# Kernel tuning notes

Hardware: AMD Instinct MI355X
Metric: run time of the kernel (lower is better)

## Reference

```python
import jax, jax.numpy as jnp
import numpy as np


def setup_inputs() -> dict:
    key = jax.random.key(0)
    k1, k2, k3, k4 = jax.random.split(key, 4)
    B, L, R, H, D = 64, 512, 512, 512, 256
    return {
        "lstm_lt": jax.random.normal(k1, (B, L, H), dtype=jnp.float32),
        "lstm_rt": jax.random.normal(k2, (B, R, H), dtype=jnp.float32),
        "atten_W": jax.random.normal(k3, (H, D), dtype=jnp.float32) * 0.05,
        "diagnoal_W": jax.random.normal(k4, (1, 1, D), dtype=jnp.float32) * 0.05,
    }


def reference(lstm_lt, lstm_rt, atten_W, diagnoal_W):
    # Projection (the original's broadcast-multiply-sum is exactly a GEMM):
    # atten_lt[b,l,d] = tanh(sum_h lstm_lt[b,l,h] * W[h,d]) * diag_W[d]
    atten_lt = jnp.tanh(jnp.einsum('blh,hd->bld', lstm_lt, atten_W)) * diagnoal_W
    atten_rt = jnp.tanh(jnp.einsum('brh,hd->brd', lstm_rt, atten_W))
    # batch_dot over the attention dim -> (B, L, R)
    atten_value = jnp.einsum('bld,brd->blr', atten_lt, atten_rt)
    # No masks supplied (len(inputs)==2 path); softmax over last axis.
    return jax.nn.softmax(atten_value, axis=-1)
```

## Files before the change

kernel.cpp:

```cpp
#include <hip/hip_runtime.h>

typedef __attribute__((ext_vector_type(8))) __bf16 bf16x8;
typedef __attribute__((ext_vector_type(4))) float f32x4;

#define DI __device__ __forceinline__

DI unsigned short f2bf(float x) {
  unsigned u = __float_as_uint(x);
  u += 0x7fffu + ((u >> 16) & 1u);
  return (unsigned short)(u >> 16);
}

DI bf16x8 cvt8(f32x4 lo, f32x4 hi) {
  bf16x8 r;
  r[0] = (__bf16)lo.x; r[1] = (__bf16)lo.y; r[2] = (__bf16)lo.z; r[3] = (__bf16)lo.w;
  r[4] = (__bf16)hi.x; r[5] = (__bf16)hi.y; r[6] = (__bf16)hi.z; r[7] = (__bf16)hi.w;
  return r;
}

DI float tanh_fast(float x) {
  float ax = fabsf(x);
  float e = __expf(-2.0f * ax);
  float t = (1.0f - e) / (1.0f + e);
  return x < 0.0f ? -t : t;
}

DI void glds16(const void* gptr, void* lptr) {
  __builtin_amdgcn_global_load_lds(
      (const __attribute__((address_space(1))) unsigned int*)gptr,
      (__attribute__((address_space(3))) unsigned int*)lptr, 16, 0, 0);
}


__global__ void k_wt(const float* __restrict__ W, unsigned short* __restrict__ Wt) {
  int n  = blockIdx.x;
  int k8 = threadIdx.x;
  unsigned v[8];
#pragma unroll
  for (int j = 0; j < 8; j++) v[j] = f2bf(W[(k8 * 8 + j) * 256 + n]);
  uint4 p;
  p.x = v[0] | (v[1] << 16);
  p.y = v[2] | (v[3] << 16);
  p.z = v[4] | (v[5] << 16);
  p.w = v[6] | (v[7] << 16);
  size_t idx = ((size_t)(n >> 4) * 16 + (k8 >> 2)) * 512 + (k8 & 3) * 128 + (n & 15) * 8;
  *(uint4*)&Wt[idx] = p;
}

__global__ __launch_bounds__(512, 4) void k_proj(
    const float* __restrict__ Alt, const float* __restrict__ Art,
    const unsigned short* __restrict__ Wt, const float* __restrict__ diag,
    unsigned short* __restrict__ Olt, unsigned short* __restrict__ Ort) {
  __shared__ __align__(16) float As[128 * 64];

  int bx = blockIdx.x;
  bool is_lt = bx < 256;
  int m0 = (is_lt ? bx : bx - 256) * 128;
  const char* Abase = (const char*)((is_lt ? Alt : Art) + (size_t)m0 * 512);
  const char* Bt = (const char*)Wt;

  int tid  = threadIdx.x;
  int lane = tid & 63;
  int wid  = tid >> 6;
  int wm   = wid >> 2;
  int wn   = wid & 3;
  int l15  = lane & 15;
  int quad = lane >> 4;
  int r7   = l15 & 7;

  int lr4 = lane >> 4, c16 = lane & 15;
  int aoff = lr4 * 2048 + ((c16 ^ lr4) << 4);

  char* AsB = (char*)As;

  f32x4 zero = {0.0f, 0.0f, 0.0f, 0.0f};
  f32x4 acc[4][4];
#pragma unroll
  for (int i = 0; i < 4; i++)
#pragma unroll
    for (int j = 0; j < 4; j++) acc[i][j] = zero;

  for (int k0 = 0; k0 < 512; k0 += 64) {
    uint4 bv[2][4];
#pragma unroll
    for (int ks = 0; ks < 2; ks++)
#pragma unroll
      for (int nt = 0; nt < 4; nt++)
        bv[ks][nt] = *(const uint4*)(
            Bt + (((size_t)(wn * 4 + nt) * 16 + (k0 >> 5) + ks) << 10) + lane * 16);

#pragma unroll
    for (int i = 0; i < 4; i++) {
      int j = wid * 4 + i;
      glds16(Abase + (size_t)j * 8192 + (size_t)k0 * 4 + (aoff ^ ((j & 1) << 6)),
             AsB + j * 1024);
    }
    __syncthreads();

#pragma unroll
    for (int ks = 0; ks < 2; ks++) {
      bf16x8 a[4];
#pragma unroll
      for (int mt = 0; mt < 4; mt++) {
        int row = wm * 64 + mt * 16 + l15;
        int c0 = ks * 8 + quad * 2;
        f32x4 lo = *(const f32x4*)(AsB + row * 256 + (((c0    ) ^ r7) << 4));
        f32x4 hi = *(const f32x4*)(AsB + row * 256 + (((c0 + 1) ^ r7) << 4));
        a[mt] = cvt8(lo, hi);
      }
      __builtin_amdgcn_s_setprio(1);
#pragma unroll
      for (int mt = 0; mt < 4; mt++)
#pragma unroll
        for (int nt = 0; nt < 4; nt++)
          acc[mt][nt] = __builtin_amdgcn_mfma_f32_16x16x32_bf16(
              a[mt], __builtin_bit_cast(bf16x8, bv[ks][nt]), acc[mt][nt], 0, 0, 0);
      __builtin_amdgcn_s_setprio(0);
    }
    __syncthreads();
  }

  float dscale[4];
#pragma unroll
  for (int nt = 0; nt < 4; nt++)
    dscale[nt] = is_lt ? diag[wn * 64 + nt * 16 + l15] : 1.0f;

  if (is_lt) {
    unsigned short* O = Olt + (size_t)m0 * 256;
#pragma unroll
    for (int mt = 0; mt < 4; mt++)
#pragma unroll
      for (int r = 0; r < 4; r++) {
        int row = wm * 64 + mt * 16 + quad * 4 + r;
#pragma unroll
        for (int nt = 0; nt < 4; nt++) {
          int col = wn * 64 + nt * 16 + l15;
          O[(size_t)row * 256 + col] = f2bf(tanh_fast(acc[mt][nt][r]) * dscale[nt]);
        }
      }
  } else {
#pragma unroll
    for (int mt = 0; mt < 4; mt++)
#pragma unroll
      for (int r = 0; r < 4; r++) {
        int row = wm * 64 + mt * 16 + quad * 4 + r;
        int m = m0 + row;
        int bb = m >> 9, rr = m & 511;
#pragma unroll
        for (int nt = 0; nt < 4; nt++) {
          int d = wn * 64 + nt * 16 + l15;
          size_t idx = (size_t)bb * 131072 +
                       ((size_t)(rr >> 4) * 8 + (d >> 5)) * 512 +
                       ((d >> 3) & 3) * 128 + (rr & 15) * 8 + (d & 7);
          Ort[idx] = f2bf(tanh_fast(acc[mt][nt][r]));
        }
      }
  }
}

__global__ __launch_bounds__(512, 4) void k_attn(
    const unsigned short* __restrict__ Lt, const unsigned short* __restrict__ Rt,
    float* __restrict__ Out) {
  __shared__ __align__(16) unsigned short Ls[64 * 256];
  __shared__ float red[8][64];
  __shared__ float rowv[64];

  int bx = blockIdx.x;
  int b  = (bx & 7) * 8 + ((bx >> 3) & 7);
  int l0 = (bx >> 6) * 64;
  const char* Lb = (const char*)(Lt + ((size_t)b * 512 + l0) * 256);
  const char* Rb = (const char*)Rt + (size_t)b * 262144;
  float* Ob = Out + ((size_t)b * 512 + l0) * 512;

  int tid  = threadIdx.x;
  int lane = tid & 63;
  int wid  = tid >> 6;
  int l15  = lane & 15;
  int quad = lane >> 4;
  int r7   = l15 & 7;

  char* LsB = (char*)Ls;

  f32x4 zero = {0.0f, 0.0f, 0.0f, 0.0f};
  f32x4 acc[4][4];
#pragma unroll
  for (int i = 0; i < 4; i++)
#pragma unroll
    for (int j = 0; j < 4; j++) acc[i][j] = zero;

#pragma unroll
  for (int i = 0; i < 4; i++) {
    int grow = wid * 8 + i * 2 + (lane >> 5);
    glds16(Lb + (size_t)grow * 512 + (((lane & 31) ^ (grow & 7)) << 4),
           LsB + (wid * 8 + i * 2) * 512 + (lane & 31) * 16 + (lane >> 5) * 512);
  }
  __syncthreads();

  for (int t = 0; t < 8; t++) {
    uint4 rv[4];
#pragma unroll
    for (int nt = 0; nt < 4; nt++)
      rv[nt] = *(const uint4*)(
          Rb + (((size_t)(wid * 4 + nt) * 8 + t) << 10) + lane * 16);
    bf16x8 a[4];
#pragma unroll
    for (int mt = 0; mt < 4; mt++) {
      int row = mt * 16 + l15;
      a[mt] = *(const bf16x8*)(LsB + row * 512 + (((t * 4 + quad) ^ r7) << 4));
    }
    __builtin_amdgcn_s_setprio(1);
#pragma unroll
    for (int mt = 0; mt < 4; mt++)
#pragma unroll
      for (int nt = 0; nt < 4; nt++)
        acc[mt][nt] = __builtin_amdgcn_mfma_f32_16x16x32_bf16(
            a[mt], __builtin_bit_cast(bf16x8, rv[nt]), acc[mt][nt], 0, 0, 0);
    __builtin_amdgcn_s_setprio(0);
  }

#pragma unroll
  for (int mt = 0; mt < 4; mt++) {
#pragma unroll
    for (int r = 0; r < 4; r++) {
      float m = fmaxf(fmaxf(acc[mt][0][r], acc[mt][1][r]),
                      fmaxf(acc[mt][2][r], acc[mt][3][r]));
      m = fmaxf(m, __shfl_xor(m, 1));
      m = fmaxf(m, __shfl_xor(m, 2));
      m = fmaxf(m, __shfl_xor(m, 4));
      m = fmaxf(m, __shfl_xor(m, 8));
      if (l15 == 0) red[wid][mt * 16 + quad * 4 + r] = m;
    }
  }
  __syncthreads();
  if (tid < 64) {
    float m = red[0][tid];
#pragma unroll
    for (int w = 1; w < 8; w++) m = fmaxf(m, red[w][tid]);
    rowv[tid] = m;
  }
  __syncthreads();

#pragma unroll
  for (int mt = 0; mt < 4; mt++) {
#pragma unroll
    for (int r = 0; r < 4; r++) {
      float base = rowv[mt * 16 + quad * 4 + r];
      float s = 0.0f;
#pragma unroll
      for (int nt = 0; nt < 4; nt++) {
        float e = __expf(acc[mt][nt][r] - base);
        acc[mt][nt][r] = e;
        s += e;
      }
      s += __shfl_xor(s, 1);
      s += __shfl_xor(s, 2);
      s += __shfl_xor(s, 4);
      s += __shfl_xor(s, 8);
      if (l15 == 0) red[wid][mt * 16 + quad * 4 + r] = s;
    }
  }
  __syncthreads();
  if (tid < 64) {
    float s = red[0][tid];
#pragma unroll
    for (int w = 1; w < 8; w++) s += red[w][tid];
    rowv[tid] = 1.0f / s;
  }
  __syncthreads();

#pragma unroll
  for (int mt = 0; mt < 4; mt++) {
#pragma unroll
    for (int r = 0; r < 4; r++) {
      int row = mt * 16 + quad * 4 + r;
      float inv = rowv[row];
#pragma unroll
      for (int nt = 0; nt < 4; nt++) {
        int col = wid * 64 + nt * 16 + l15;
        Ob[(size_t)row * 512 + col] = acc[mt][nt][r] * inv;
      }
    }
  }
}

extern "C" void kernel_launch(void* const* d_in, const int* in_sizes, int n_in,
                              void* d_out, int out_size, void* d_ws, size_t ws_size,
                              hipStream_t stream) {
  const float* lstm_lt = (const float*)d_in[0];
  const float* lstm_rt = (const float*)d_in[1];
  const float* W       = (const float*)d_in[2];
  const float* diag    = (const float*)d_in[3];
  float* out = (float*)d_out;

  unsigned short* Wt  = (unsigned short*)d_ws;
  unsigned short* Olt = (unsigned short*)((char*)d_ws + (size_t)256 * 512 * 2);
  unsigned short* Ort = Olt + (size_t)32768 * 256;

  k_wt<<<dim3(256), dim3(64), 0, stream>>>(W, Wt);
  k_proj<<<dim3(512), dim3(512), 0, stream>>>(lstm_lt, lstm_rt, Wt, diag, Olt, Ort);
  k_attn<<<dim3(512), dim3(512), 0, stream>>>(Olt, Ort, out);
}
```

Baseline: 217.1 us.

## Drop LDS staging; load MFMA fragments directly from global memory in both GEMMs

The projection kernel no longer stages fp32 A tiles in LDS with global_load_lds and barriers. Each lane now reads its MFMA A-fragment straight from global memory, converts it to bf16, and unrolls the K loop by two. The left projection output is now written in the same MFMA-fragment-packed layout as the right one, so the attention kernel can read its L operand directly from global memory instead of staging it in LDS. This removes barriers and shared-memory traffic and lowers the occupancy hint to 2. The cost is more global/L2 traffic, since waves sharing rows in a block reload the same A data, plus higher register pressure.

```diff
diff --git a/kernel.cpp b/kernel.cpp
--- a/kernel.cpp
+++ b/kernel.cpp
@@ -23,12 +23,6 @@
   float e = __expf(-2.0f * ax);
   float t = (1.0f - e) / (1.0f + e);
   return x < 0.0f ? -t : t;
-}
-
-DI void glds16(const void* gptr, void* lptr) {
-  __builtin_amdgcn_global_load_lds(
-      (const __attribute__((address_space(1))) unsigned int*)gptr,
-      (__attribute__((address_space(3))) unsigned int*)lptr, 16, 0, 0);
 }
 
 
@@ -47,17 +41,16 @@
   *(uint4*)&Wt[idx] = p;
 }
 
-__global__ __launch_bounds__(512, 4) void k_proj(
+__global__ __launch_bounds__(512, 2) void k_proj(
     const float* __restrict__ Alt, const float* __restrict__ Art,
     const unsigned short* __restrict__ Wt, const float* __restrict__ diag,
     unsigned short* __restrict__ Olt, unsigned short* __restrict__ Ort) {
-  __shared__ __align__(16) float As[128 * 64];
-
   int bx = blockIdx.x;
   bool is_lt = bx < 256;
   int m0 = (is_lt ? bx : bx - 256) * 128;
   const char* Abase = (const char*)((is_lt ? Alt : Art) + (size_t)m0 * 512);
   const char* Bt = (const char*)Wt;
+  unsigned short* O = is_lt ? Olt : Ort;
 
   int tid  = threadIdx.x;
   int lane = tid & 63;
@@ -66,12 +59,6 @@
   int wn   = wid & 3;
   int l15  = lane & 15;
   int quad = lane >> 4;
-  int r7   = l15 & 7;
-
-  int lr4 = lane >> 4, c16 = lane & 15;
-  int aoff = lr4 * 2048 + ((c16 ^ lr4) << 4);
-
-  char* AsB = (char*)As;
 
   f32x4 zero = {0.0f, 0.0f, 0.0f, 0.0f};
   f32x4 acc[4][4];
@@ -80,44 +67,37 @@
 #pragma unroll
     for (int j = 0; j < 4; j++) acc[i][j] = zero;
 
-  for (int k0 = 0; k0 < 512; k0 += 64) {
+  const char* Arow = Abase + (size_t)(wm * 64 + l15) * 2048 + quad * 32;
+
+#pragma unroll 2
+  for (int t = 0; t < 8; t++) {
     uint4 bv[2][4];
 #pragma unroll
     for (int ks = 0; ks < 2; ks++)
 #pragma unroll
       for (int nt = 0; nt < 4; nt++)
         bv[ks][nt] = *(const uint4*)(
-            Bt + (((size_t)(wn * 4 + nt) * 16 + (k0 >> 5) + ks) << 10) + lane * 16);
-
-#pragma unroll
-    for (int i = 0; i < 4; i++) {
-      int j = wid * 4 + i;
-      glds16(Abase + (size_t)j * 8192 + (size_t)k0 * 4 + (aoff ^ ((j & 1) << 6)),
-             AsB + j * 1024);
-    }
-    __syncthreads();
-
-#pragma unroll
-    for (int ks = 0; ks < 2; ks++) {
-      bf16x8 a[4];
+            Bt + (((size_t)(wn * 4 + nt) * 16 + t * 2 + ks) << 10) + lane * 16);
+
+    bf16x8 a[2][4];
+#pragma unroll
+    for (int ks = 0; ks < 2; ks++)
 #pragma unroll
       for (int mt = 0; mt < 4; mt++) {
-        int row = wm * 64 + mt * 16 + l15;
-        int c0 = ks * 8 + quad * 2;
-        f32x4 lo = *(const f32x4*)(AsB + row * 256 + (((c0    ) ^ r7) << 4));
-        f32x4 hi = *(const f32x4*)(AsB + row * 256 + (((c0 + 1) ^ r7) << 4));
-        a[mt] = cvt8(lo, hi);
-      }
-      __builtin_amdgcn_s_setprio(1);
+        const char* ap = Arow + (size_t)mt * 32768 + t * 256 + ks * 128;
+        f32x4 lo = *(const f32x4*)(ap);
+        f32x4 hi = *(const f32x4*)(ap + 16);
+        a[ks][mt] = cvt8(lo, hi);
+      }
+
+#pragma unroll
+    for (int ks = 0; ks < 2; ks++)
 #pragma unroll
       for (int mt = 0; mt < 4; mt++)
 #pragma unroll
         for (int nt = 0; nt < 4; nt++)
           acc[mt][nt] = __builtin_amdgcn_mfma_f32_16x16x32_bf16(
-              a[mt], __builtin_bit_cast(bf16x8, bv[ks][nt]), acc[mt][nt], 0, 0, 0);
-      __builtin_amdgcn_s_setprio(0);
-    }
-    __syncthreads();
+              a[ks][mt], __builtin_bit_cast(bf16x8, bv[ks][nt]), acc[mt][nt], 0, 0, 0);
   }
 
   float dscale[4];
@@ -125,50 +105,33 @@
   for (int nt = 0; nt < 4; nt++)
     dscale[nt] = is_lt ? diag[wn * 64 + nt * 16 + l15] : 1.0f;
 
-  if (is_lt) {
-    unsigned short* O = Olt + (size_t)m0 * 256;
-#pragma unroll
-    for (int mt = 0; mt < 4; mt++)
-#pragma unroll
-      for (int r = 0; r < 4; r++) {
-        int row = wm * 64 + mt * 16 + quad * 4 + r;
-#pragma unroll
-        for (int nt = 0; nt < 4; nt++) {
-          int col = wn * 64 + nt * 16 + l15;
-          O[(size_t)row * 256 + col] = f2bf(tanh_fast(acc[mt][nt][r]) * dscale[nt]);
-        }
-      }
-  } else {
-#pragma unroll
-    for (int mt = 0; mt < 4; mt++)
-#pragma unroll
-      for (int r = 0; r < 4; r++) {
-        int row = wm * 64 + mt * 16 + quad * 4 + r;
-        int m = m0 + row;
-        int bb = m >> 9, rr = m & 511;
-#pragma unroll
-        for (int nt = 0; nt < 4; nt++) {
-          int d = wn * 64 + nt * 16 + l15;
-          size_t idx = (size_t)bb * 131072 +
-                       ((size_t)(rr >> 4) * 8 + (d >> 5)) * 512 +
-                       ((d >> 3) & 3) * 128 + (rr & 15) * 8 + (d & 7);
-          Ort[idx] = f2bf(tanh_fast(acc[mt][nt][r]));
-        }
-      }
-  }
+#pragma unroll
+  for (int mt = 0; mt < 4; mt++)
+#pragma unroll
+    for (int r = 0; r < 4; r++) {
+      int m = m0 + wm * 64 + mt * 16 + quad * 4 + r;
+      int bb = m >> 9, rr = m & 511;
+#pragma unroll
+      for (int nt = 0; nt < 4; nt++) {
+        int d = wn * 64 + nt * 16 + l15;
+        size_t idx = (size_t)bb * 131072 +
+                     ((size_t)(rr >> 4) * 8 + (d >> 5)) * 512 +
+                     ((d >> 3) & 3) * 128 + (rr & 15) * 8 + (d & 7);
+        O[idx] = f2bf(tanh_fast(acc[mt][nt][r]) * dscale[nt]);
+      }
+    }
 }
 
 __global__ __launch_bounds__(512, 4) void k_attn(
     const unsigned short* __restrict__ Lt, const unsigned short* __restrict__ Rt,
     float* __restrict__ Out) {
-  __shared__ __align__(16) unsigned short Ls[64 * 256];
   __shared__ float red[8][64];
   __shared__ float rowv[64];
 
   int bx = blockIdx.x;
   int b  = (bx & 7) * 8 + ((bx >> 3) & 7);
   int l0 = (bx >> 6) * 64;
-  const char* Lb = (const char*)(Lt + ((size_t)b * 512 + l0) * 256);
+  const char* Lb = (const char*)Lt + (size_t)b * 262144;
   const char* Rb = (const char*)Rt + (size_t)b * 262144;
   float* Ob = Out + ((size_t)b * 512 + l0) * 512;
 
@@ -177,9 +140,6 @@
   int wid  = tid >> 6;
   int l15  = lane & 15;
   int quad = lane >> 4;
-  int r7   = l15 & 7;
-
-  char* LsB = (char*)Ls;
 
   f32x4 zero = {0.0f, 0.0f, 0.0f, 0.0f};
   f32x4 acc[4][4];
@@ -188,34 +148,23 @@
 #pragma unroll
     for (int j = 0; j < 4; j++) acc[i][j] = zero;
 
-#pragma unroll
-  for (int i = 0; i < 4; i++) {
-    int grow = wid * 8 + i * 2 + (lane >> 5);
-    glds16(Lb + (size_t)grow * 512 + (((lane & 31) ^ (grow & 7)) << 4),
-           LsB + (wid * 8 + i * 2) * 512 + (lane & 31) * 16 + (lane >> 5) * 512);
-  }
-  __syncthreads();
+  int lrow = l0 >> 4;
 
   for (int t = 0; t < 8; t++) {
-    uint4 rv[4];
+    uint4 av[4], rv[4];
+#pragma unroll
+    for (int mt = 0; mt < 4; mt++)
+      av[mt] = *(const uint4*)(Lb + (((size_t)(lrow + mt) * 8 + t) << 10) + lane * 16);
 #pragma unroll
     for (int nt = 0; nt < 4; nt++)
-      rv[nt] = *(const uint4*)(
-          Rb + (((size_t)(wid * 4 + nt) * 8 + t) << 10) + lane * 16);
-    bf16x8 a[4];
-#pragma unroll
-    for (int mt = 0; mt < 4; mt++) {
-      int row = mt * 16 + l15;
-      a[mt] = *(const bf16x8*)(LsB + row * 512 + (((t * 4 + quad) ^ r7) << 4));
-    }
-    __builtin_amdgcn_s_setprio(1);
+      rv[nt] = *(const uint4*)(Rb + (((size_t)(wid * 4 + nt) * 8 + t) << 10) + lane * 16);
 #pragma unroll
     for (int mt = 0; mt < 4; mt++)
 #pragma unroll
       for (int nt = 0; nt < 4; nt++)
         acc[mt][nt] = __builtin_amdgcn_mfma_f32_16x16x32_bf16(
-            a[mt], __builtin_bit_cast(bf16x8, rv[nt]), acc[mt][nt], 0, 0, 0);
-    __builtin_amdgcn_s_setprio(0);
+            __builtin_bit_cast(bf16x8, av[mt]),
+            __builtin_bit_cast(bf16x8, rv[nt]), acc[mt][nt], 0, 0, 0);
   }
 
 #pragma unroll
```

After: 257.7 us. 1.19x slower.
